# Optimization experiments

Hardware: AMD Instinct MI355X
Metric: run time of the kernel (lower is better)

Reference implementation:

```python
import jax, jax.numpy as jnp
import numpy as np

D = 800  # embed dim == GRU units (hardcoded in module)


def gru_scan(x, h0, W, U, b):
    """Keras GRU, reset_after=True, activation=tanh, recurrent_activation=softmax.
    x: [B,T,D_in], h0: [B,H], W: [D_in,3H], U: [H,3H], b: [2,3H] (input bias, recurrent bias).
    Gate order: z, r, h (Keras convention). Returns (seq [B,T,H], last state [B,H])."""
    H = h0.shape[-1]
    # Precompute input projections for all timesteps (big fused GEMM).
    xg = jnp.einsum('btd,dk->btk', x, W) + b[0]          # [B,T,3H]
    xg = jnp.swapaxes(xg, 0, 1)                          # [T,B,3H]
    br = b[1]

    def step(h, xt):
        rec = h @ U + br                                 # [B,3H]
        rz, rr, rh = rec[:, :H], rec[:, H:2 * H], rec[:, 2 * H:]
        xz, xr, xh = xt[:, :H], xt[:, H:2 * H], xt[:, 2 * H:]
        z = jax.nn.softmax(xz + rz, axis=-1)             # recurrent_activation='softmax'
        r = jax.nn.softmax(xr + rr, axis=-1)
        hh = jnp.tanh(xh + r * rh)                       # reset_after: r applied after recurrent matmul
        hn = z * h + (1.0 - z) * hh
        return hn, hn

    hT, ys = jax.lax.scan(step, h0, xg)
    return jnp.swapaxes(ys, 0, 1), hT


def setup_inputs() -> dict:
    key = jax.random.key(0)
    ks = jax.random.split(key, 16)
    Vf, Ve, B, T = 30000, 32000, 64, 48
    s = 0.05

    def n(k, shape):
        return jax.random.normal(k, shape, jnp.float32) * s

    return {
        'encoder_input': jax.random.randint(ks[0], (B, T), 0, Vf),
        'decoder_input': jax.random.randint(ks[1], (B, T), 0, Ve),
        'emb_fr': n(ks[2], (Vf, D)),
        'W_d1': n(ks[3], (D, D)), 'b_d1': jnp.zeros((D,), jnp.float32),
        'Wf1': n(ks[4], (D, 3 * D)), 'Uf1': n(ks[5], (D, 3 * D)), 'bf1': jnp.zeros((2, 3 * D), jnp.float32),
        'Wf2': n(ks[6], (D, 3 * D)), 'Uf2': n(ks[7], (D, 3 * D)), 'bf2': jnp.zeros((2, 3 * D), jnp.float32),
        'emb_en': n(ks[8], (Ve, D)),
        'We1': n(ks[9], (D, 3 * D)), 'Ue1': n(ks[10], (D, 3 * D)), 'be1': jnp.zeros((2, 3 * D), jnp.float32),
        'We2': n(ks[11], (D, 3 * D)), 'Ue2': n(ks[12], (D, 3 * D)), 'be2': jnp.zeros((2, 3 * D), jnp.float32),
        'W_out': n(ks[13], (D, Ve)), 'b_out': jnp.zeros((Ve,), jnp.float32),
    }


def reference(encoder_input, decoder_input, emb_fr, W_d1, b_d1,
              Wf1, Uf1, bf1, Wf2, Uf2, bf2, emb_en,
              We1, Ue1, be1, We2, Ue2, be2, W_out, b_out):
    fe = emb_fr[encoder_input]                           # [B,Tf,D]
    fe = jax.nn.relu(fe @ W_d1 + b_d1)
    ee = emb_en[decoder_input]                           # [B,Te,D]
    B = encoder_input.shape[0]
    h0 = jnp.zeros((B, D), dtype=fe.dtype)
    g1, h1 = gru_scan(fe, h0, Wf1, Uf1, bf1)
    g2, h2 = gru_scan(g1, h1, Wf2, Uf2, bf2)
    e1, h3 = gru_scan(ee, h2, We1, Ue1, be1)
    e2, h4 = gru_scan(e1, h3, We2, Ue2, be2)
    logits = e2 @ W_out + b_out                          # [B,Te,Ve]
    return jax.nn.softmax(logits, axis=-1)
```

## Files before the change

### kernel.cpp

```cpp
#include <hip/hip_runtime.h>

#define DD 800
#define HH 800
#define BB 64
#define TT 48
#define N3H 2400
#define VV 32000
#define MR (TT*BB)
#define NBLK 25

typedef __attribute__((ext_vector_type(8))) short bf16x8;
typedef __attribute__((ext_vector_type(4))) float f32x4;
typedef __attribute__((ext_vector_type(4))) float float4v;
typedef __attribute__((address_space(1))) const unsigned int as1_uint;
typedef __attribute__((address_space(3))) unsigned int as3_uint;

__device__ __forceinline__ short f2bf(float f) {
  unsigned int u = __builtin_bit_cast(unsigned int, f);
  u = (u + 0x7fffu + ((u >> 16) & 1u)) >> 16;
  return (short)(unsigned short)u;
}

__device__ __forceinline__ void gload16(const void* g, void* l) {
  __builtin_amdgcn_global_load_lds((as1_uint*)g, (as3_uint*)l, 16, 0, 0);
}

__device__ __forceinline__ void store16_cc(short* p, bf16x8 v) {
  asm volatile("global_store_dwordx4 %0, %1, off sc0 sc1" :: "v"(p), "v"(v));
}

__global__ void k_cast_transpose(const float* __restrict__ src, short* __restrict__ dst,
                                 int K, int N) {
  __shared__ float tile[32][33];
  int n0 = blockIdx.x * 32, k0 = blockIdx.y * 32;
  int tx = threadIdx.x, ty = threadIdx.y;
#pragma unroll
  for (int i = 0; i < 4; ++i) {
    int k = k0 + ty + i * 8, n = n0 + tx;
    if (k < K && n < N) tile[ty + i * 8][tx] = src[(size_t)k * N + n];
  }
  __syncthreads();
#pragma unroll
  for (int i = 0; i < 4; ++i) {
    int n = n0 + ty + i * 8, k = k0 + tx;
    if (n < N && k < K) dst[(size_t)n * K + k] = f2bf(tile[tx][ty + i * 8]);
  }
}

__global__ void k_gather(const int* __restrict__ ids, const float* __restrict__ emb,
                         short* __restrict__ out) {
  int r = blockIdx.x;
  int t = r >> 6, b = r & 63;
  int id = ids[b * TT + t];
  int i = threadIdx.x;
  if (i < 100) {
    const float* s = emb + (size_t)id * DD + i * 8;
    float4v v0 = *(const float4v*)s;
    float4v v1 = *(const float4v*)(s + 4);
    bf16x8 o;
    o[0] = f2bf(v0[0]); o[1] = f2bf(v0[1]); o[2] = f2bf(v0[2]); o[3] = f2bf(v0[3]);
    o[4] = f2bf(v1[0]); o[5] = f2bf(v1[1]); o[6] = f2bf(v1[2]); o[7] = f2bf(v1[3]);
    *(bf16x8*)(out + (size_t)r * DD + i * 8) = o;
  }
}

template <int EPI>
__global__ __launch_bounds__(256) void k_gemm(const short* __restrict__ A,
                                              const short* __restrict__ BT,
                                              const float* __restrict__ bias,
                                              float* __restrict__ Cf,
                                              short* __restrict__ Cb,
                                              int N, int K, int ldc) {
  __shared__ short lA[128 * 32];
  __shared__ short lB[128 * 32];
  const int tid = threadIdx.x, wid = tid >> 6, lane = tid & 63;
  const int m0 = blockIdx.y * 128, n0 = blockIdx.x * 128;
  const int wr = wid >> 1, wc = wid & 1;
  f32x4 acc[4][4] = {};
  for (int kt = 0; kt < K / 32; ++kt) {
    const int kb = kt * 32;
#pragma unroll
    for (int rr = 0; rr < 2; ++rr) {
      int s = rr * 256 + tid;
      gload16(A + (size_t)(m0 + (s >> 2)) * K + kb + (s & 3) * 8, (char*)lA + s * 16);
      gload16(BT + (size_t)(n0 + (s >> 2)) * K + kb + (s & 3) * 8, (char*)lB + s * 16);
    }
    __syncthreads();
    bf16x8 af[4], bfr[4];
#pragma unroll
    for (int i = 0; i < 4; ++i)
      af[i] = *(const bf16x8*)(lA + (wr * 64 + i * 16 + (lane & 15)) * 32 + (lane >> 4) * 8);
#pragma unroll
    for (int j = 0; j < 4; ++j)
      bfr[j] = *(const bf16x8*)(lB + (wc * 64 + j * 16 + (lane & 15)) * 32 + (lane >> 4) * 8);
#pragma unroll
    for (int i = 0; i < 4; ++i)
#pragma unroll
      for (int j = 0; j < 4; ++j)
        acc[i][j] = __builtin_amdgcn_mfma_f32_16x16x32_bf16(af[i], bfr[j], acc[i][j], 0, 0, 0);
    __syncthreads();
  }
  const int hi = lane >> 4, ccol = lane & 15;
#pragma unroll
  for (int i = 0; i < 4; ++i) {
    int row = m0 + wr * 64 + i * 16 + hi * 4;
#pragma unroll
    for (int j = 0; j < 4; ++j) {
      int col = n0 + wc * 64 + j * 16 + ccol;
      if (col >= N) continue;
      float bv = bias ? bias[col] : 0.f;
#pragma unroll
      for (int rg = 0; rg < 4; ++rg) {
        int r = row + rg;
        float v = acc[i][j][rg] + bv;
        if (EPI == 0) Cf[(size_t)r * ldc + col] = v;
        else          Cb[(size_t)r * ldc + col] = f2bf(v < 0.f ? 0.f : v);
      }
    }
  }
}

__device__ __forceinline__ void bar_sync(int* flags, int ep, int tid) {
  asm volatile("s_waitcnt vmcnt(0)" ::: "memory");
  __syncthreads();
  if (tid == 0)
    __hip_atomic_store(&flags[blockIdx.x * 32], ep, __ATOMIC_RELAXED, __HIP_MEMORY_SCOPE_AGENT);
  if (tid < 64) {
    bool ok;
    do {
      int v = ep;
      if (tid < NBLK)
        v = __hip_atomic_load(&flags[tid * 32], __ATOMIC_RELAXED, __HIP_MEMORY_SCOPE_AGENT);
      ok = __all(v - ep >= 0);
      if (!ok) __builtin_amdgcn_s_sleep(1);
    } while (!ok);
  }
  __syncthreads();
}

template <int HEPI>
__global__ __launch_bounds__(512, 1) void k_fused(
    const float* __restrict__ xg, const short* __restrict__ UT,
    const float* __restrict__ br, float* __restrict__ hF,
    const short* __restrict__ hInit, short* __restrict__ hSeq,
    float* __restrict__ Spart, int* __restrict__ flags, int ep0,
    const short* __restrict__ gA, const short* __restrict__ gBT,
    const float* __restrict__ gbias, float* __restrict__ gCf,
    float* __restrict__ gPp, int gN, int gldc, int gNT, int gNtiles,
    int* __restrict__ tcnt, int pollBase) {
  __shared__ __align__(16) char smem[159744];
  const int tid = threadIdx.x, wid = tid >> 6, lane = tid & 63;
  const int hi = lane >> 4, ccol = lane & 15;

  if (blockIdx.x < NBLK) {
    short* uT    = (short*)smem;
    float* sSum  = (float*)(smem + 155136);
    short* hTile = (short*)(smem + 155648);
    const int bid = blockIdx.x, c0 = bid * 32;
    const int rt = wid & 3, ch = wid >> 2;
    for (int idx = tid; idx < 96 * 100; idx += 512) {
      int rr = idx / 100, chk = idx % 100;
      int grow = (rr >> 5) * HH + c0 + (rr & 31);
      *(bf16x8*)(uT + rr * 808 + chk * 8) = *(const bf16x8*)(UT + (size_t)grow * HH + chk * 8);
    }
    const int crow = rt * 16 + hi * 4;
    const int gcol = c0 + ch * 16 + ccol;
    const int arow = rt * 16 + ccol;
    const short* uz = uT + (0 * 32 + ch * 16 + ccol) * 808;
    const short* ur = uT + (1 * 32 + ch * 16 + ccol) * 808;
    const short* uh = uT + (2 * 32 + ch * 16 + ccol) * 808;
    f32x4 hfr;
#pragma unroll
    for (int rg = 0; rg < 4; ++rg) hfr[rg] = hF[(crow + rg) * HH + gcol];
    const float brz = br[gcol], brr = br[HH + gcol], brh = br[2 * HH + gcol];
    int ep = ep0;
    float xzv[4], xrv[4], xhv[4];
#pragma unroll
    for (int rg = 0; rg < 4; ++rg) {
      const float* xrow = xg + ((size_t)(crow + rg)) * N3H;
      xzv[rg] = xrow[gcol];
      xrv[rg] = xrow[HH + gcol];
      xhv[rg] = xrow[2 * HH + gcol];
    }
    __syncthreads();

#pragma unroll 1
    for (int t = 0; t < TT; ++t) {
      const short* hPrev = (t == 0) ? hInit : hSeq + (size_t)(t - 1) * BB * HH;
      bf16x8 areg[25];
#pragma unroll
      for (int kt = 0; kt < 25; ++kt)
        areg[kt] = *(const bf16x8*)(hPrev + arow * HH + kt * 32 + hi * 8);
      f32x4 az = {}, ar = {}, ah = {};
#pragma unroll
      for (int kt = 0; kt < 25; ++kt) {
        const int o = kt * 32 + hi * 8;
        az = __builtin_amdgcn_mfma_f32_16x16x32_bf16(areg[kt], *(const bf16x8*)(uz + o), az, 0, 0, 0);
        ar = __builtin_amdgcn_mfma_f32_16x16x32_bf16(areg[kt], *(const bf16x8*)(ur + o), ar, 0, 0, 0);
        ah = __builtin_amdgcn_mfma_f32_16x16x32_bf16(areg[kt], *(const bf16x8*)(uh + o), ah, 0, 0, 0);
      }
      float ez[4], er[4], rh[4];
      float* sb = Spart + (size_t)t * 50 * 128;
#pragma unroll
      for (int rg = 0; rg < 4; ++rg) {
        ez[rg] = __expf(xzv[rg] + az[rg] + brz);
        er[rg] = __expf(xrv[rg] + ar[rg] + brr);
        rh[rg] = ah[rg] + brh;
        float s1 = ez[rg], s2 = er[rg];
#pragma unroll
        for (int mm = 1; mm < 16; mm <<= 1) {
          s1 += __shfl_xor(s1, mm);
          s2 += __shfl_xor(s2, mm);
        }
        if (ccol == 0) {
          const int slot = bid * 2 + ch;
          __hip_atomic_store(&sb[slot * 128 + crow + rg], s1, __ATOMIC_RELAXED, __HIP_MEMORY_SCOPE_AGENT);
          __hip_atomic_store(&sb[slot * 128 + 64 + crow + rg], s2, __ATOMIC_RELAXED, __HIP_MEMORY_SCOPE_AGENT);
        }
      }
      bar_sync(flags, ++ep, tid);
      if (tid < 128) {
        float s = 0.f;
#pragma unroll
        for (int sl = 0; sl < 2 * NBLK; ++sl)
          s += __hip_atomic_load(&sb[sl * 128 + tid], __ATOMIC_RELAXED, __HIP_MEMORY_SCOPE_AGENT);
        sSum[tid] = s;
      }
      __syncthreads();
#pragma unroll
      for (int rg = 0; rg < 4; ++rg) {
        int r = crow + rg;
        float z = ez[rg] / sSum[r];
        float rr2 = er[rg] / sSum[64 + r];
        float hh = tanhf(xhv[rg] + rr2 * rh[rg]);
        float hn = z * hfr[rg] + (1.f - z) * hh;
        hfr[rg] = hn;
        hTile[r * 32 + ch * 16 + ccol] = f2bf(hn);
      }
      __syncthreads();
      short* hCur = hSeq + (size_t)t * BB * HH;
      if (tid < 256) {
        int row = tid >> 2, seg = tid & 3;
        store16_cc(hCur + row * HH + c0 + seg * 8, *(const bf16x8*)(hTile + row * 32 + seg * 8));
      }
      if (t + 1 < TT) {
#pragma unroll
        for (int rg = 0; rg < 4; ++rg) {
          const float* xrow = xg + ((size_t)(t + 1) * BB + crow + rg) * N3H;
          xzv[rg] = xrow[gcol];
          xrv[rg] = xrow[HH + gcol];
          xhv[rg] = xrow[2 * HH + gcol];
        }
      }
      bar_sync(flags, ++ep, tid);
    }
#pragma unroll
    for (int rg = 0; rg < 4; ++rg) hF[(crow + rg) * HH + gcol] = hfr[rg];
    return;
  }

  short* lA = (short*)smem;
  short* lB = (short*)(smem + 8192);
  int*   tk = (int*)(smem + 16384);
  const int wr = wid >> 1, wc = wid & 1;
  for (;;) {
    if (tid == 0)
      tk[0] = __hip_atomic_fetch_add(tcnt, 1, __ATOMIC_RELAXED, __HIP_MEMORY_SCOPE_AGENT);
    __syncthreads();
    const int t0 = tk[0];
    if (t0 >= gNtiles) break;
    const int mb = t0 / gNT, nb = t0 % gNT;
    const int m0 = mb * 128, n0 = nb * 128;
    {
      int tmax = 2 * mb + 1; if (tmax > TT - 1) tmax = TT - 1;
      const int ft = pollBase + 2 * tmax + 2;
      bool ok;
      do {
        int v = ft;
        if (lane < NBLK)
          v = __hip_atomic_load(&flags[lane * 32], __ATOMIC_RELAXED, __HIP_MEMORY_SCOPE_AGENT);
        ok = __all(v - ft >= 0);
        if (!ok) __builtin_amdgcn_s_sleep(2);
      } while (!ok);
      asm volatile("" ::: "memory");
    }
    f32x4 acc[2][4] = {};
    const int srow = tid >> 2, sseg = tid & 3;
    for (int kt = 0; kt < 25; ++kt) {
      const int kb = kt * 32;
      gload16(gA + (size_t)(m0 + srow) * 800 + kb + sseg * 8, (char*)lA + tid * 16);
      gload16(gBT + (size_t)(n0 + srow) * 800 + kb + sseg * 8, (char*)lB + tid * 16);
      __syncthreads();
      bf16x8 af[2], bf[4];
#pragma unroll
      for (int i = 0; i < 2; ++i)
        af[i] = *(const bf16x8*)(lA + (wr * 32 + i * 16 + (lane & 15)) * 32 + hi * 8);
#pragma unroll
      for (int j = 0; j < 4; ++j)
        bf[j] = *(const bf16x8*)(lB + (wc * 64 + j * 16 + (lane & 15)) * 32 + hi * 8);
#pragma unroll
      for (int i = 0; i < 2; ++i)
#pragma unroll
        for (int j = 0; j < 4; ++j)
          acc[i][j] = __builtin_amdgcn_mfma_f32_16x16x32_bf16(af[i], bf[j], acc[i][j], 0, 0, 0);
      __syncthreads();
    }
    if (HEPI == 2) {
#pragma unroll
      for (int i = 0; i < 2; ++i) {
        int row = m0 + wr * 32 + i * 16 + hi * 4;
#pragma unroll
        for (int rg = 0; rg < 4; ++rg) {
          int r = row + rg;
          int orow = (r & 63) * TT + (r >> 6);
          float part = 0.f;
#pragma unroll
          for (int j = 0; j < 4; ++j) {
            int col = n0 + wc * 64 + j * 16 + ccol;
            float v = __expf(acc[i][j][rg] + gbias[col]);
            part += v;
            gCf[(size_t)orow * gldc + col] = v;
          }
#pragma unroll
          for (int mm = 1; mm < 16; mm <<= 1) part += __shfl_xor(part, mm);
          if (ccol == 0) gPp[(size_t)orow * 512 + nb * 2 + wc] = part;
        }
      }
    } else {
#pragma unroll
      for (int i = 0; i < 2; ++i) {
        int row = m0 + wr * 32 + i * 16 + hi * 4;
#pragma unroll
        for (int j = 0; j < 4; ++j) {
          int col = n0 + wc * 64 + j * 16 + ccol;
          if (col >= gN) continue;
          float bv = gbias[col];
#pragma unroll
          for (int rg = 0; rg < 4; ++rg)
            gCf[(size_t)(row + rg) * gldc + col] = acc[i][j][rg] + bv;
        }
      }
    }
  }
}

__global__ __launch_bounds__(256) void k_softmax(float* __restrict__ out,
                                                 const float* __restrict__ Pp) {
  float* row = out + (size_t)blockIdx.x * VV;
  const float* pp = Pp + (size_t)blockIdx.x * 512;
  const int tid = threadIdx.x;
  __shared__ float red[4];
  float sum = 0.f;
  for (int i = tid; i < 500; i += 256) sum += pp[i];
#pragma unroll
  for (int s = 32; s >= 1; s >>= 1) sum += __shfl_xor(sum, s);
  if ((tid & 63) == 0) red[tid >> 6] = sum;
  __syncthreads();
  float inv = 1.f / (red[0] + red[1] + red[2] + red[3]);
  for (int i = tid * 4; i < VV; i += 1024) {
    float4v v = *(const float4v*)(row + i);
    v[0] *= inv; v[1] *= inv; v[2] *= inv; v[3] *= inv;
    *(float4v*)(row + i) = v;
  }
}

extern "C" void kernel_launch(void* const* d_in, const int* in_sizes, int n_in,
                              void* d_out, int out_size, void* d_ws, size_t ws_size,
                              hipStream_t stream) {
  (void)in_sizes; (void)n_in; (void)out_size; (void)ws_size;
  const int*   enc  = (const int*)d_in[0];
  const int*   dec  = (const int*)d_in[1];
  const float* embF = (const float*)d_in[2];
  const float* Wd1  = (const float*)d_in[3];
  const float* bd1  = (const float*)d_in[4];
  const float* Wf1  = (const float*)d_in[5];
  const float* Uf1  = (const float*)d_in[6];
  const float* bf1  = (const float*)d_in[7];
  const float* Wf2  = (const float*)d_in[8];
  const float* Uf2  = (const float*)d_in[9];
  const float* bf2  = (const float*)d_in[10];
  const float* embE = (const float*)d_in[11];
  const float* We1  = (const float*)d_in[12];
  const float* Ue1  = (const float*)d_in[13];
  const float* be1  = (const float*)d_in[14];
  const float* We2  = (const float*)d_in[15];
  const float* Ue2  = (const float*)d_in[16];
  const float* be2  = (const float*)d_in[17];
  const float* Wout = (const float*)d_in[18];
  const float* bout = (const float*)d_in[19];

  char* p = (char*)d_ws;
  auto alloc = [&](size_t bytes) { char* r = p; p += (bytes + 255) & ~(size_t)255; return r; };
  short* WdT = (short*)alloc((size_t)896 * 800 * 2);
  short* WTb[4]; short* UTb[4];
  for (int i = 0; i < 4; ++i) {
    WTb[i] = (short*)alloc((size_t)2432 * 800 * 2);
    UTb[i] = (short*)alloc((size_t)2400 * 800 * 2);
  }
  short* WoT = (short*)alloc((size_t)VV * 800 * 2);
  short* feA = (short*)alloc((size_t)MR * DD * 2);
  short* fe  = (short*)alloc((size_t)MR * DD * 2);
  short* ee  = (short*)alloc((size_t)MR * DD * 2);
  short* g1  = (short*)alloc((size_t)MR * HH * 2);
  short* g2s = (short*)alloc((size_t)MR * HH * 2);
  short* e1  = (short*)alloc((size_t)MR * HH * 2);
  short* e2  = (short*)alloc((size_t)MR * HH * 2);
  float* xgA = (float*)alloc((size_t)MR * N3H * 4);
  float* xgB = (float*)alloc((size_t)MR * N3H * 4);
  float* Ppart = (float*)alloc((size_t)MR * 512 * 4);
  float* Spart = (float*)alloc((size_t)TT * 50 * 128 * 4);
  float* hF   = (float*)alloc((size_t)BB * HH * 4);
  short* hIn0 = (short*)alloc((size_t)BB * HH * 2);
  int* flags  = (int*)alloc((size_t)NBLK * 32 * 4);
  int* tcnt   = (int*)alloc((size_t)16 * 4);

  size_t tail = (char*)(tcnt + 16) - (char*)hF;
  hipMemsetAsync(hF, 0, tail, stream);

  dim3 tb(32, 8);
  k_cast_transpose<<<dim3(25, 25), tb, 0, stream>>>(Wd1, WdT, 800, 800);
  const float* Ws[4] = {Wf1, Wf2, We1, We2};
  const float* Us[4] = {Uf1, Uf2, Ue1, Ue2};
  for (int i = 0; i < 4; ++i) {
    k_cast_transpose<<<dim3(75, 25), tb, 0, stream>>>(Ws[i], WTb[i], 800, 2400);
    k_cast_transpose<<<dim3(75, 25), tb, 0, stream>>>(Us[i], UTb[i], 800, 2400);
  }
  k_cast_transpose<<<dim3(1000, 25), tb, 0, stream>>>(Wout, WoT, 800, VV);
  k_gather<<<MR, 128, 0, stream>>>(enc, embF, feA);
  k_gather<<<MR, 128, 0, stream>>>(dec, embE, ee);
  k_gemm<1><<<dim3(7, 24), 256, 0, stream>>>(feA, WdT, bd1, nullptr, fe, 800, 800, 800);
  k_gemm<0><<<dim3(19, 24), 256, 0, stream>>>(fe, WTb[0], bf1, xgA, nullptr, N3H, 800, N3H);

  const float* bs[4] = {bf1, bf2, be1, be2};
  short* hSeqL[4] = {g1, g2s, e1, e2};
  float* xgR[4] = {xgA, xgB, xgA, xgB};
  const short* hA[4]   = {g1, ee, e1, e2};
  const short* hBT[4]  = {WTb[1], WTb[2], WTb[3], WoT};
  const float* hBias[4]= {bs[1], bs[2], bs[3], bout};
  float* hOut[4] = {xgB, xgA, xgB, (float*)d_out};
  int   hPoll[4] = {0 * 96, -1000000, 2 * 96, 3 * 96};

  for (int l = 0; l < 4; ++l) {
    const short* hInit = (l == 0) ? hIn0 : hSeqL[l - 1] + (size_t)(TT - 1) * BB * HH;
    if (l < 3) {
      k_fused<0><<<256, 512, 0, stream>>>(xgR[l], UTb[l], bs[l] + N3H, hF, hInit, hSeqL[l],
                                          Spart, flags, l * 2 * TT,
                                          hA[l], hBT[l], hBias[l], hOut[l], nullptr,
                                          N3H, N3H, 19, 24 * 19, &tcnt[l], hPoll[l]);
    } else {
      k_fused<2><<<256, 512, 0, stream>>>(xgR[l], UTb[l], bs[l] + N3H, hF, hInit, hSeqL[l],
                                          Spart, flags, l * 2 * TT,
                                          hA[l], hBT[l], hBias[l], hOut[l], Ppart,
                                          VV, VV, 250, 24 * 250, &tcnt[l], hPoll[l]);
    }
  }
  k_softmax<<<MR, 256, 0, stream>>>((float*)d_out, Ppart);
}
```

Measured before the change: 2.369 ms.

## Replace per-step grid barriers with data-sentinel polling in recurrent GRU kernel

Removes the two flag-based grid barriers per timestep. Consumers now spin on the data itself: hidden-state buffers are pre-filled with 0xFF sentinels and re-read until no word equals -1, and the softmax partial sums are polled until every slot is nonzero. A per-layer done counter gates the overlapped GEMM tiles. This is meant to cut barrier latency on the serial recurrence, but it relies on the sentinel values never occurring in real data (for example, an exp sum being exactly zero). It also adds bounded retry loops that could silently proceed with stale data.

```diff
diff --git a/kernel.cpp b/kernel.cpp
--- a/kernel.cpp
+++ b/kernel.cpp
@@ -12,6 +12,7 @@
 typedef __attribute__((ext_vector_type(8))) short bf16x8;
 typedef __attribute__((ext_vector_type(4))) float f32x4;
 typedef __attribute__((ext_vector_type(4))) float float4v;
+typedef __attribute__((ext_vector_type(4))) int int4v;
 typedef __attribute__((address_space(1))) const unsigned int as1_uint;
 typedef __attribute__((address_space(3))) unsigned int as3_uint;
 
@@ -27,6 +28,11 @@
 
 __device__ __forceinline__ void store16_cc(short* p, bf16x8 v) {
   asm volatile("global_store_dwordx4 %0, %1, off sc0 sc1" :: "v"(p), "v"(v));
+}
+__device__ __forceinline__ bf16x8 load16_cc_nw(const short* p) {
+  bf16x8 v;
+  asm volatile("global_load_dwordx4 %0, %1, off sc0 sc1" : "=&v"(v) : "v"(p));
+  return v;
 }
 
 __global__ void k_cast_transpose(const float* __restrict__ src, short* __restrict__ dst,
@@ -120,34 +126,16 @@
   }
 }
 
-__device__ __forceinline__ void bar_sync(int* flags, int ep, int tid) {
-  asm volatile("s_waitcnt vmcnt(0)" ::: "memory");
-  __syncthreads();
-  if (tid == 0)
-    __hip_atomic_store(&flags[blockIdx.x * 32], ep, __ATOMIC_RELAXED, __HIP_MEMORY_SCOPE_AGENT);
-  if (tid < 64) {
-    bool ok;
-    do {
-      int v = ep;
-      if (tid < NBLK)
-        v = __hip_atomic_load(&flags[tid * 32], __ATOMIC_RELAXED, __HIP_MEMORY_SCOPE_AGENT);
-      ok = __all(v - ep >= 0);
-      if (!ok) __builtin_amdgcn_s_sleep(1);
-    } while (!ok);
-  }
-  __syncthreads();
-}
-
 template <int HEPI>
 __global__ __launch_bounds__(512, 1) void k_fused(
     const float* __restrict__ xg, const short* __restrict__ UT,
     const float* __restrict__ br, float* __restrict__ hF,
     const short* __restrict__ hInit, short* __restrict__ hSeq,
-    float* __restrict__ Spart, int* __restrict__ flags, int ep0,
+    float* __restrict__ SpartL, int* __restrict__ wDone,
     const short* __restrict__ gA, const short* __restrict__ gBT,
     const float* __restrict__ gbias, float* __restrict__ gCf,
     float* __restrict__ gPp, int gN, int gldc, int gNT, int gNtiles,
-    int* __restrict__ tcnt, int pollBase) {
+    int* __restrict__ tcnt, const int* __restrict__ hGate) {
   __shared__ __align__(16) char smem[159744];
   const int tid = threadIdx.x, wid = tid >> 6, lane = tid & 63;
   const int hi = lane >> 4, ccol = lane & 15;
@@ -173,7 +161,6 @@
 #pragma unroll
     for (int rg = 0; rg < 4; ++rg) hfr[rg] = hF[(crow + rg) * HH + gcol];
     const float brz = br[gcol], brr = br[HH + gcol], brh = br[2 * HH + gcol];
-    int ep = ep0;
     float xzv[4], xrv[4], xhv[4];
 #pragma unroll
     for (int rg = 0; rg < 4; ++rg) {
@@ -188,9 +175,25 @@
     for (int t = 0; t < TT; ++t) {
       const short* hPrev = (t == 0) ? hInit : hSeq + (size_t)(t - 1) * BB * HH;
       bf16x8 areg[25];
-#pragma unroll
-      for (int kt = 0; kt < 25; ++kt)
-        areg[kt] = *(const bf16x8*)(hPrev + arow * HH + kt * 32 + hi * 8);
+      {
+        bool ok; int guard = 0;
+        do {
+#pragma unroll
+          for (int kt = 0; kt < 25; ++kt)
+            areg[kt] = load16_cc_nw(hPrev + arow * HH + kt * 32 + hi * 8);
+          asm volatile("s_waitcnt vmcnt(0)" ::: "memory");
+          __builtin_amdgcn_sched_barrier(0);
+          int bad = 0;
+#pragma unroll
+          for (int kt = 0; kt < 25; ++kt) {
+            int4v w = __builtin_bit_cast(int4v, areg[kt]);
+            bad |= (w.x == -1) | (w.y == -1) | (w.z == -1) | (w.w == -1);
+          }
+          ok = __all(bad == 0);
+          if (!ok) __builtin_amdgcn_s_sleep(1);
+        } while (!ok && ++guard < (1 << 18));
+      }
+      __builtin_amdgcn_sched_barrier(0);
       f32x4 az = {}, ar = {}, ah = {};
 #pragma unroll
       for (int kt = 0; kt < 25; ++kt) {
@@ -200,7 +203,7 @@
         ah = __builtin_amdgcn_mfma_f32_16x16x32_bf16(areg[kt], *(const bf16x8*)(uh + o), ah, 0, 0, 0);
       }
       float ez[4], er[4], rh[4];
-      float* sb = Spart + (size_t)t * 50 * 128;
+      float* sb = SpartL + (size_t)t * 50 * 128;
 #pragma unroll
       for (int rg = 0; rg < 4; ++rg) {
         ez[rg] = __expf(xzv[rg] + az[rg] + brz);
@@ -218,12 +221,18 @@
           __hip_atomic_store(&sb[slot * 128 + 64 + crow + rg], s2, __ATOMIC_RELAXED, __HIP_MEMORY_SCOPE_AGENT);
         }
       }
-      bar_sync(flags, ++ep, tid);
       if (tid < 128) {
-        float s = 0.f;
-#pragma unroll
-        for (int sl = 0; sl < 2 * NBLK; ++sl)
-          s += __hip_atomic_load(&sb[sl * 128 + tid], __ATOMIC_RELAXED, __HIP_MEMORY_SCOPE_AGENT);
+        bool ok; int guard = 0; float s;
+        do {
+          s = 0.f; ok = true;
+#pragma unroll
+          for (int sl = 0; sl < 2 * NBLK; ++sl) {
+            float v = __hip_atomic_load(&sb[sl * 128 + tid], __ATOMIC_RELAXED, __HIP_MEMORY_SCOPE_AGENT);
+            ok &= (v != 0.f);
+            s += v;
+          }
+          if (!ok) __builtin_amdgcn_s_sleep(1);
+        } while (!ok && ++guard < (1 << 18));
         sSum[tid] = s;
       }
       __syncthreads();
@@ -243,6 +252,10 @@
         int row = tid >> 2, seg = tid & 3;
         store16_cc(hCur + row * HH + c0 + seg * 8, *(const bf16x8*)(hTile + row * 32 + seg * 8));
       }
+      asm volatile("s_waitcnt vmcnt(0)" ::: "memory");
+      __syncthreads();
+      if (tid == 0)
+        __hip_atomic_fetch_add(wDone, 1, __ATOMIC_RELAXED, __HIP_MEMORY_SCOPE_AGENT);
       if (t + 1 < TT) {
 #pragma unroll
         for (int rg = 0; rg < 4; ++rg) {
@@ -252,7 +265,6 @@
           xhv[rg] = xrow[2 * HH + gcol];
         }
       }
-      bar_sync(flags, ++ep, tid);
     }
 #pragma unroll
     for (int rg = 0; rg < 4; ++rg) hF[(crow + rg) * HH + gcol] = hfr[rg];
@@ -271,18 +283,18 @@
     if (t0 >= gNtiles) break;
     const int mb = t0 / gNT, nb = t0 % gNT;
     const int m0 = mb * 128, n0 = nb * 128;
-    {
-      int tmax = 2 * mb + 1; if (tmax > TT - 1) tmax = TT - 1;
-      const int ft = pollBase + 2 * tmax + 2;
-      bool ok;
-      do {
-        int v = ft;
-        if (lane < NBLK)
-          v = __hip_atomic_load(&flags[lane * 32], __ATOMIC_RELAXED, __HIP_MEMORY_SCOPE_AGENT);
-        ok = __all(v - ft >= 0);
-        if (!ok) __builtin_amdgcn_s_sleep(2);
-      } while (!ok);
-      asm volatile("" ::: "memory");
+    if (hGate) {
+      if (tid == 0) {
+        int tmax = 2 * mb + 1; if (tmax > TT - 1) tmax = TT - 1;
+        const int tgt = NBLK * (tmax + 1);
+        bool ok; int guard = 0;
+        do {
+          int v = __hip_atomic_load((int*)hGate, __ATOMIC_RELAXED, __HIP_MEMORY_SCOPE_AGENT);
+          ok = (v - tgt >= 0);
+          if (!ok) __builtin_amdgcn_s_sleep(2);
+        } while (!ok && ++guard < (1 << 20));
+      }
+      __syncthreads();
     }
     f32x4 acc[2][4] = {};
     const int srow = tid >> 2, sseg = tid & 3;
@@ -408,14 +420,14 @@
   float* xgA = (float*)alloc((size_t)MR * N3H * 4);
   float* xgB = (float*)alloc((size_t)MR * N3H * 4);
   float* Ppart = (float*)alloc((size_t)MR * 512 * 4);
-  float* Spart = (float*)alloc((size_t)TT * 50 * 128 * 4);
+  float* Spart = (float*)alloc((size_t)4 * TT * 50 * 128 * 4);
   float* hF   = (float*)alloc((size_t)BB * HH * 4);
   short* hIn0 = (short*)alloc((size_t)BB * HH * 2);
-  int* flags  = (int*)alloc((size_t)NBLK * 32 * 4);
+  int* hDone  = (int*)alloc((size_t)16 * 4);
   int* tcnt   = (int*)alloc((size_t)16 * 4);
 
-  size_t tail = (char*)(tcnt + 16) - (char*)hF;
-  hipMemsetAsync(hF, 0, tail, stream);
+  hipMemsetAsync(Spart, 0, (char*)(tcnt + 16) - (char*)Spart, stream);
+  hipMemsetAsync(g1, 0xFF, (char*)(e2 + (size_t)MR * HH) - (char*)g1, stream);
 
   dim3 tb(32, 8);
   k_cast_transpose<<<dim3(25, 25), tb, 0, stream>>>(Wd1, WdT, 800, 800);
@@ -434,24 +446,25 @@
   const float* bs[4] = {bf1, bf2, be1, be2};
   short* hSeqL[4] = {g1, g2s, e1, e2};
   float* xgR[4] = {xgA, xgB, xgA, xgB};
-  const short* hA[4]   = {g1, ee, e1, e2};
-  const short* hBT[4]  = {WTb[1], WTb[2], WTb[3], WoT};
-  const float* hBias[4]= {bs[1], bs[2], bs[3], bout};
+  const short* hA[4]    = {g1, ee, e1, e2};
+  const short* hBT[4]   = {WTb[1], WTb[2], WTb[3], WoT};
+  const float* hBias[4] = {bs[1], bs[2], bs[3], bout};
   float* hOut[4] = {xgB, xgA, xgB, (float*)d_out};
-  int   hPoll[4] = {0 * 96, -1000000, 2 * 96, 3 * 96};
+  const int* hGate[4] = {&hDone[0], nullptr, &hDone[2], &hDone[3]};
 
   for (int l = 0; l < 4; ++l) {
     const short* hInit = (l == 0) ? hIn0 : hSeqL[l - 1] + (size_t)(TT - 1) * BB * HH;
+    float* SpL = Spart + (size_t)l * TT * 50 * 128;
     if (l < 3) {
       k_fused<0><<<256, 512, 0, stream>>>(xgR[l], UTb[l], bs[l] + N3H, hF, hInit, hSeqL[l],
-                                          Spart, flags, l * 2 * TT,
+                                          SpL, &hDone[l],
                                           hA[l], hBT[l], hBias[l], hOut[l], nullptr,
-                                          N3H, N3H, 19, 24 * 19, &tcnt[l], hPoll[l]);
+                                          N3H, N3H, 19, 24 * 19, &tcnt[l], hGate[l]);
     } else {
       k_fused<2><<<256, 512, 0, stream>>>(xgR[l], UTb[l], bs[l] + N3H, hF, hInit, hSeqL[l],
-                                          Spart, flags, l * 2 * TT,
+                                          SpL, &hDone[l],
                                           hA[l], hBT[l], hBias[l], hOut[l], Ppart,
-                                          VV, VV, 250, 24 * 250, &tcnt[l], hPoll[l]);
+                                          VV, VV, 250, 24 * 250, &tcnt[l], hGate[l]);
     }
   }
   k_softmax<<<MR, 256, 0, stream>>>((float*)d_out, Ppart);
```

After: 2.706 ms. +14.2%, slower.
